# Performance work log

Hardware: AMD Instinct MI355X
Metric: run time of the kernel (lower is better)

The kernel has to match this reference:

```python
import jax, jax.numpy as jnp
import numpy as np


def _trilinear_sample(src, iz, iy, ix):
    """grid_sample 3D, mode='bilinear' (trilinear), padding_mode='zeros', on unnormalized voxel coords.
    src: [B,C,D,H,W]; iz,iy,ix: [B,D,H,W] float voxel coords (iz indexes D, iy H, ix W)."""
    B, C, D, H, W = src.shape
    z0 = jnp.floor(iz); y0 = jnp.floor(iy); x0 = jnp.floor(ix)
    tz = iz - z0; ty = iy - y0; tx = ix - x0
    z0i = z0.astype(jnp.int32); y0i = y0.astype(jnp.int32); x0i = x0.astype(jnp.int32)
    src_flat = src.reshape(B, C, D * H * W)

    def corner(dz, dy, dx):
        zc = z0i + dz; yc = y0i + dy; xc = x0i + dx
        valid = (zc >= 0) & (zc < D) & (yc >= 0) & (yc < H) & (xc >= 0) & (xc < W)
        zcc = jnp.clip(zc, 0, D - 1); ycc = jnp.clip(yc, 0, H - 1); xcc = jnp.clip(xc, 0, W - 1)
        lin = (zcc * H + ycc) * W + xcc                      # [B,D,H,W] flat spatial index
        vals = jax.vmap(lambda v, i: v[:, i.ravel()])(src_flat, lin)  # [B,C,D*H*W]
        vals = vals.reshape(B, C, D, H, W)
        wz = tz if dz else (1.0 - tz)
        wy = ty if dy else (1.0 - ty)
        wx = tx if dx else (1.0 - tx)
        w = (wz * wy * wx) * valid.astype(src.dtype)         # zeros padding
        return vals * w[:, None]

    out = jnp.zeros_like(src)
    for dz in (0, 1):
        for dy in (0, 1):
            for dx in (0, 1):
                out = out + corner(dz, dy, dx)
    return out


def reference(src, flow):
    B, _, D, H, W = flow.shape
    dt = flow.dtype
    # identity grid, channels ordered (z,y,x) i.e. (D,H,W), matching torch.meshgrid indexing='ij'
    gz, gy, gx = jnp.meshgrid(jnp.arange(D, dtype=dt), jnp.arange(H, dtype=dt),
                              jnp.arange(W, dtype=dt), indexing='ij')
    grid = jnp.stack([gz, gy, gx])[None]                     # [1,3,D,H,W]
    coords = grid + flow                                      # absolute voxel coords
    denom = jnp.array([D - 1, H - 1, W - 1], dtype=dt).reshape(1, 3, 1, 1, 1)
    norm = 2.0 * (coords / denom - 0.5)                       # normalized to [-1,1]
    # grid_sample expects last-dim order (x,y,z); align_corners=True unnormalization:
    ix = (norm[:, 2] + 1.0) * (W - 1) * 0.5
    iy = (norm[:, 1] + 1.0) * (H - 1) * 0.5
    iz = (norm[:, 0] + 1.0) * (D - 1) * 0.5
    return _trilinear_sample(src, iz, iy, ix)


def setup_inputs() -> dict:
    key = jax.random.key(0)
    k1, k2 = jax.random.split(key)
    B, C, D, H, W = 2, 2, 128, 160, 128
    src = jax.random.normal(k1, (B, C, D, H, W), dtype=jnp.float32)
    flow = jax.random.normal(k2, (B, 3, D, H, W), dtype=jnp.float32)
    return {"src": src, "flow": flow}
```

## Files before the change

kernel.cpp:

```cpp
#include <hip/hip_runtime.h>


#define B_ 2
#define C_ 2
#define D_ 128
#define H_ 160
#define W_ 128
constexpr int S_ = D_ * H_ * W_;

#define ZT 8
#define YT 8
#define XT 32
#define RZ 3
#define RY 3
#define RX 4
#define CZ (ZT + 2 * RZ)
#define CY (YT + 2 * RY)
#define CX (XT + 2 * RX)
#define NTHREADS 512
#define PLANE (CZ * CY * CX)
#define CHPP (PLANE / 4)
#define NCHUNK_TOT (2 * CHPP)

typedef const __attribute__((address_space(1))) unsigned int ga_u32;
typedef __attribute__((address_space(3))) unsigned int lds_u32;

__device__ __forceinline__ void gload16(const float* g, float* l) {
    __builtin_amdgcn_global_load_lds((ga_u32*)g, (lds_u32*)l, 16, 0, 0);
}

__device__ __forceinline__ float2 compute_pair(
    int x, int y, int z, float fz, float fy, float fx,
    int zb, int yb, int xb,
    int zlo, int zhi, int ylo, int yhi, int xlo, int xhi,
    const float* __restrict__ tile, const float* __restrict__ s0)
{
    const float iz = (float)z + fz;
    const float iy = (float)y + fy;
    const float ix = (float)x + fx;

    const float zf = floorf(iz), yf = floorf(iy), xf = floorf(ix);
    const float tz = iz - zf, ty = iy - yf, tx = ix - xf;
    const int z0 = (int)zf, y0 = (int)yf, x0 = (int)xf;

    const int zc0 = min(max(z0, 0), D_ - 1), zc1 = min(max(z0 + 1, 0), D_ - 1);
    const int yc0 = min(max(y0, 0), H_ - 1), yc1 = min(max(y0 + 1, 0), H_ - 1);
    const int xp  = min(max(x0, 0), W_ - 2);

    const float wz0 = ((unsigned)z0       < (unsigned)D_) ? (1.f - tz) : 0.f;
    const float wz1 = ((unsigned)(z0 + 1) < (unsigned)D_) ? tz         : 0.f;
    const float wy0 = ((unsigned)y0       < (unsigned)H_) ? (1.f - ty) : 0.f;
    const float wy1 = ((unsigned)(y0 + 1) < (unsigned)H_) ? ty         : 0.f;
    const float wx0 = ((unsigned)x0       < (unsigned)W_) ? (1.f - tx) : 0.f;
    const float wx1 = ((unsigned)(x0 + 1) < (unsigned)W_) ? tx         : 0.f;
    const bool hi0 = x0 > xp;
    const bool lo1 = x0 < xp;

    const bool fast = (zc0 >= zlo) & (zc1 < zhi) &
                      (yc0 >= ylo) & (yc1 < yhi) &
                      (xp >= xlo) & (xp + 1 < xhi);

    float acc0, acc1;
    if (fast) {
        const int izl0 = zc0 - (zb - RZ), izl1 = zc1 - (zb - RZ);
        const int iyl0 = yc0 - (yb - RY), iyl1 = yc1 - (yb - RY);
        const int ixl  = xp - (xb - RX);
        const int o00 = (izl0 * CY + iyl0) * CX + ixl;
        const int o01 = (izl0 * CY + iyl1) * CX + ixl;
        const int o10 = (izl1 * CY + iyl0) * CX + ixl;
        const int o11 = (izl1 * CY + iyl1) * CX + ixl;
        const float a00 = tile[o00],         b00 = tile[o00 + 1];
        const float a01 = tile[o01],         b01 = tile[o01 + 1];
        const float a10 = tile[o10],         b10 = tile[o10 + 1];
        const float a11 = tile[o11],         b11 = tile[o11 + 1];
        const float c00 = tile[PLANE + o00], d00 = tile[PLANE + o00 + 1];
        const float c01 = tile[PLANE + o01], d01 = tile[PLANE + o01 + 1];
        const float c10 = tile[PLANE + o10], d10 = tile[PLANE + o10 + 1];
        const float c11 = tile[PLANE + o11], d11 = tile[PLANE + o11 + 1];
        const float q00 = wx0 * (hi0 ? b00 : a00) + wx1 * (lo1 ? a00 : b00);
        const float q01 = wx0 * (hi0 ? b01 : a01) + wx1 * (lo1 ? a01 : b01);
        const float q10 = wx0 * (hi0 ? b10 : a10) + wx1 * (lo1 ? a10 : b10);
        const float q11 = wx0 * (hi0 ? b11 : a11) + wx1 * (lo1 ? a11 : b11);
        const float r00 = wx0 * (hi0 ? d00 : c00) + wx1 * (lo1 ? c00 : d00);
        const float r01 = wx0 * (hi0 ? d01 : c01) + wx1 * (lo1 ? c01 : d01);
        const float r10 = wx0 * (hi0 ? d10 : c10) + wx1 * (lo1 ? c10 : d10);
        const float r11 = wx0 * (hi0 ? d11 : c11) + wx1 * (lo1 ? c11 : d11);
        acc0 = wz0 * (wy0 * q00 + wy1 * q01) + wz1 * (wy0 * q10 + wy1 * q11);
        acc1 = wz0 * (wy0 * r00 + wy1 * r01) + wz1 * (wy0 * r10 + wy1 * r11);
    } else {
        const int l00 = (zc0 * H_ + yc0) * W_ + xp;
        const int l01 = (zc0 * H_ + yc1) * W_ + xp;
        const int l10 = (zc1 * H_ + yc0) * W_ + xp;
        const int l11 = (zc1 * H_ + yc1) * W_ + xp;
        const float a00 = s0[l00],      b00 = s0[l00 + 1];
        const float a01 = s0[l01],      b01 = s0[l01 + 1];
        const float a10 = s0[l10],      b10 = s0[l10 + 1];
        const float a11 = s0[l11],      b11 = s0[l11 + 1];
        const float c00 = s0[S_ + l00], d00 = s0[S_ + l00 + 1];
        const float c01 = s0[S_ + l01], d01 = s0[S_ + l01 + 1];
        const float c10 = s0[S_ + l10], d10 = s0[S_ + l10 + 1];
        const float c11 = s0[S_ + l11], d11 = s0[S_ + l11 + 1];
        const float q00 = wx0 * (hi0 ? b00 : a00) + wx1 * (lo1 ? a00 : b00);
        const float q01 = wx0 * (hi0 ? b01 : a01) + wx1 * (lo1 ? a01 : b01);
        const float q10 = wx0 * (hi0 ? b10 : a10) + wx1 * (lo1 ? a10 : b10);
        const float q11 = wx0 * (hi0 ? b11 : a11) + wx1 * (lo1 ? a11 : b11);
        const float r00 = wx0 * (hi0 ? d00 : c00) + wx1 * (lo1 ? c00 : d00);
        const float r01 = wx0 * (hi0 ? d01 : c01) + wx1 * (lo1 ? c01 : d01);
        const float r10 = wx0 * (hi0 ? d10 : c10) + wx1 * (lo1 ? c10 : d10);
        const float r11 = wx0 * (hi0 ? d11 : c11) + wx1 * (lo1 ? c11 : d11);
        acc0 = wz0 * (wy0 * q00 + wy1 * q01) + wz1 * (wy0 * q10 + wy1 * q11);
        acc1 = wz0 * (wy0 * r00 + wy1 * r01) + wz1 * (wy0 * r10 + wy1 * r11);
    }
    return make_float2(acc0, acc1);
}

__global__ __launch_bounds__(NTHREADS, 4) void warp3d_tile(
    const float* __restrict__ src,
    const float* __restrict__ flow,
    float* __restrict__ out)
{
    __shared__ float tile[2 * PLANE];

    const int tid = threadIdx.x;
    const int xb = blockIdx.x * XT;
    const int yb = blockIdx.y * YT;
    const int bz = blockIdx.z;
    const int zb = (bz & 15) * ZT;
    const int b  = bz >> 4;

    const float* fb = flow + (long long)b * 3 * S_;
    const float* s0 = src + (long long)b * C_ * S_;
    float* o0       = out + (long long)b * C_ * S_;

#pragma unroll
    for (int j = 0; j < 8; ++j) {
        const int lin = j * NTHREADS + tid;
        if (lin < NCHUNK_TOT) {
            const int pl  = (lin >= CHPP) ? 1 : 0;
            const int rem = lin - pl * CHPP;
            const int row = rem / 10;
            const int cq  = rem - row * 10;
            const int rz = row / CY, ry = row - rz * CY;
            const int gz = min(max(zb - RZ + rz, 0), D_ - 1);
            const int gy = min(max(yb - RY + ry, 0), H_ - 1);
            const int gx = min(max(xb - RX + cq * 4, 0), W_ - 4);
            gload16(s0 + pl * S_ + (gz * H_ + gy) * W_ + gx, &tile[lin * 4]);
        }
    }

    const int xq = tid & 7;
    const int ly = (tid >> 3) & 7;
    const int lz = tid >> 6;
    const int x0g = xb + xq * 4;
    const int y = yb + ly, z = zb + lz;
    const int sbase = (z * H_ + y) * W_ + x0g;
    const float4 fz4 = *(const float4*)(fb + sbase);
    const float4 fy4 = *(const float4*)(fb + S_ + sbase);
    const float4 fx4 = *(const float4*)(fb + 2 * S_ + sbase);

    __syncthreads();

    const int zlo = max(0, zb - RZ), zhi = min(D_, zb + ZT + RZ);
    const int ylo = max(0, yb - RY), yhi = min(H_, yb + YT + RY);
    const int xlo = max(0, xb - RX), xhi = min(W_, xb + XT + RX);

    const float2 v0 = compute_pair(x0g + 0, y, z, fz4.x, fy4.x, fx4.x,
                                   zb, yb, xb, zlo, zhi, ylo, yhi, xlo, xhi, tile, s0);
    const float2 v1 = compute_pair(x0g + 1, y, z, fz4.y, fy4.y, fx4.y,
                                   zb, yb, xb, zlo, zhi, ylo, yhi, xlo, xhi, tile, s0);
    const float2 v2 = compute_pair(x0g + 2, y, z, fz4.z, fy4.z, fx4.z,
                                   zb, yb, xb, zlo, zhi, ylo, yhi, xlo, xhi, tile, s0);
    const float2 v3 = compute_pair(x0g + 3, y, z, fz4.w, fy4.w, fx4.w,
                                   zb, yb, xb, zlo, zhi, ylo, yhi, xlo, xhi, tile, s0);

    *(float4*)(o0 + sbase)      = make_float4(v0.x, v1.x, v2.x, v3.x);
    *(float4*)(o0 + S_ + sbase) = make_float4(v0.y, v1.y, v2.y, v3.y);
}

extern "C" void kernel_launch(void* const* d_in, const int* in_sizes, int n_in,
                              void* d_out, int out_size, void* d_ws, size_t ws_size,
                              hipStream_t stream) {
    const float* src  = (const float*)d_in[0];
    const float* flow = (const float*)d_in[1];
    float* out = (float*)d_out;

    dim3 grid(W_ / XT, H_ / YT, (D_ / ZT) * B_);
    warp3d_tile<<<grid, NTHREADS, 0, stream>>>(src, flow, out);
}
```

Baseline: 153.2 us.

## Split channel halo loads and overlap second-channel LDS fill with first-channel compute

The two source channels are now staged into LDS with separate async global-to-LDS batches, each padded to 8192 floats. The kernel waits only for the first channel's batch (and the flow loads), then computes and stores channel 0 while channel 1 is still arriving. The per-voxel setup (weights, offsets, fast-path flag) moves into a shared state struct and is reused across both channels. In exchange it relies on hand-written vmcnt counts that assume in-order completion of memory ops, and it uses slightly more LDS per block.

```diff
diff --git a/kernel.cpp b/kernel.cpp
--- a/kernel.cpp
+++ b/kernel.cpp
@@ -18,9 +18,7 @@
 #define CY (YT + 2 * RY)
 #define CX (XT + 2 * RX)
 #define NTHREADS 512
-#define PLANE (CZ * CY * CX)
-#define CHPP (PLANE / 4)
-#define NCHUNK_TOT (2 * CHPP)
+#define PLANE_PAD 8192
 
 typedef const __attribute__((address_space(1))) unsigned int ga_u32;
 typedef __attribute__((address_space(3))) unsigned int lds_u32;
@@ -29,11 +27,16 @@
     __builtin_amdgcn_global_load_lds((ga_u32*)g, (lds_u32*)l, 16, 0, 0);
 }
 
-__device__ __forceinline__ float2 compute_pair(
+struct PState {
+    int o00, o01, o10, o11;
+    float w00, w01, w10, w11, wx0, wx1;
+    bool hi0, lo1, fast;
+};
+
+__device__ __forceinline__ PState mk_state(
     int x, int y, int z, float fz, float fy, float fx,
     int zb, int yb, int xb,
-    int zlo, int zhi, int ylo, int yhi, int xlo, int xhi,
-    const float* __restrict__ tile, const float* __restrict__ s0)
+    int zlo, int zhi, int ylo, int yhi, int xlo, int xhi)
 {
     const float iz = (float)z + fz;
     const float iy = (float)y + fy;
@@ -51,67 +54,55 @@
     const float wz1 = ((unsigned)(z0 + 1) < (unsigned)D_) ? tz         : 0.f;
     const float wy0 = ((unsigned)y0       < (unsigned)H_) ? (1.f - ty) : 0.f;
     const float wy1 = ((unsigned)(y0 + 1) < (unsigned)H_) ? ty         : 0.f;
-    const float wx0 = ((unsigned)x0       < (unsigned)W_) ? (1.f - tx) : 0.f;
-    const float wx1 = ((unsigned)(x0 + 1) < (unsigned)W_) ? tx         : 0.f;
-    const bool hi0 = x0 > xp;
-    const bool lo1 = x0 < xp;
-
-    const bool fast = (zc0 >= zlo) & (zc1 < zhi) &
-                      (yc0 >= ylo) & (yc1 < yhi) &
-                      (xp >= xlo) & (xp + 1 < xhi);
-
-    float acc0, acc1;
-    if (fast) {
+
+    PState st;
+    st.wx0 = ((unsigned)x0       < (unsigned)W_) ? (1.f - tx) : 0.f;
+    st.wx1 = ((unsigned)(x0 + 1) < (unsigned)W_) ? tx         : 0.f;
+    st.hi0 = x0 > xp;
+    st.lo1 = x0 < xp;
+    st.w00 = wz0 * wy0; st.w01 = wz0 * wy1;
+    st.w10 = wz1 * wy0; st.w11 = wz1 * wy1;
+    st.fast = (zc0 >= zlo) & (zc1 < zhi) &
+              (yc0 >= ylo) & (yc1 < yhi) &
+              (xp >= xlo) & (xp + 1 < xhi);
+    if (st.fast) {
         const int izl0 = zc0 - (zb - RZ), izl1 = zc1 - (zb - RZ);
         const int iyl0 = yc0 - (yb - RY), iyl1 = yc1 - (yb - RY);
         const int ixl  = xp - (xb - RX);
-        const int o00 = (izl0 * CY + iyl0) * CX + ixl;
-        const int o01 = (izl0 * CY + iyl1) * CX + ixl;
-        const int o10 = (izl1 * CY + iyl0) * CX + ixl;
-        const int o11 = (izl1 * CY + iyl1) * CX + ixl;
-        const float a00 = tile[o00],         b00 = tile[o00 + 1];
-        const float a01 = tile[o01],         b01 = tile[o01 + 1];
-        const float a10 = tile[o10],         b10 = tile[o10 + 1];
-        const float a11 = tile[o11],         b11 = tile[o11 + 1];
-        const float c00 = tile[PLANE + o00], d00 = tile[PLANE + o00 + 1];
-        const float c01 = tile[PLANE + o01], d01 = tile[PLANE + o01 + 1];
-        const float c10 = tile[PLANE + o10], d10 = tile[PLANE + o10 + 1];
-        const float c11 = tile[PLANE + o11], d11 = tile[PLANE + o11 + 1];
-        const float q00 = wx0 * (hi0 ? b00 : a00) + wx1 * (lo1 ? a00 : b00);
-        const float q01 = wx0 * (hi0 ? b01 : a01) + wx1 * (lo1 ? a01 : b01);
-        const float q10 = wx0 * (hi0 ? b10 : a10) + wx1 * (lo1 ? a10 : b10);
-        const float q11 = wx0 * (hi0 ? b11 : a11) + wx1 * (lo1 ? a11 : b11);
-        const float r00 = wx0 * (hi0 ? d00 : c00) + wx1 * (lo1 ? c00 : d00);
-        const float r01 = wx0 * (hi0 ? d01 : c01) + wx1 * (lo1 ? c01 : d01);
-        const float r10 = wx0 * (hi0 ? d10 : c10) + wx1 * (lo1 ? c10 : d10);
-        const float r11 = wx0 * (hi0 ? d11 : c11) + wx1 * (lo1 ? c11 : d11);
-        acc0 = wz0 * (wy0 * q00 + wy1 * q01) + wz1 * (wy0 * q10 + wy1 * q11);
-        acc1 = wz0 * (wy0 * r00 + wy1 * r01) + wz1 * (wy0 * r10 + wy1 * r11);
+        st.o00 = (izl0 * CY + iyl0) * CX + ixl;
+        st.o01 = (izl0 * CY + iyl1) * CX + ixl;
+        st.o10 = (izl1 * CY + iyl0) * CX + ixl;
+        st.o11 = (izl1 * CY + iyl1) * CX + ixl;
     } else {
-        const int l00 = (zc0 * H_ + yc0) * W_ + xp;
-        const int l01 = (zc0 * H_ + yc1) * W_ + xp;
-        const int l10 = (zc1 * H_ + yc0) * W_ + xp;
-        const int l11 = (zc1 * H_ + yc1) * W_ + xp;
-        const float a00 = s0[l00],      b00 = s0[l00 + 1];
-        const float a01 = s0[l01],      b01 = s0[l01 + 1];
-        const float a10 = s0[l10],      b10 = s0[l10 + 1];
-        const float a11 = s0[l11],      b11 = s0[l11 + 1];
-        const float c00 = s0[S_ + l00], d00 = s0[S_ + l00 + 1];
-        const float c01 = s0[S_ + l01], d01 = s0[S_ + l01 + 1];
-        const float c10 = s0[S_ + l10], d10 = s0[S_ + l10 + 1];
-        const float c11 = s0[S_ + l11], d11 = s0[S_ + l11 + 1];
-        const float q00 = wx0 * (hi0 ? b00 : a00) + wx1 * (lo1 ? a00 : b00);
-        const float q01 = wx0 * (hi0 ? b01 : a01) + wx1 * (lo1 ? a01 : b01);
-        const float q10 = wx0 * (hi0 ? b10 : a10) + wx1 * (lo1 ? a10 : b10);
-        const float q11 = wx0 * (hi0 ? b11 : a11) + wx1 * (lo1 ? a11 : b11);
-        const float r00 = wx0 * (hi0 ? d00 : c00) + wx1 * (lo1 ? c00 : d00);
-        const float r01 = wx0 * (hi0 ? d01 : c01) + wx1 * (lo1 ? c01 : d01);
-        const float r10 = wx0 * (hi0 ? d10 : c10) + wx1 * (lo1 ? c10 : d10);
-        const float r11 = wx0 * (hi0 ? d11 : c11) + wx1 * (lo1 ? c11 : d11);
-        acc0 = wz0 * (wy0 * q00 + wy1 * q01) + wz1 * (wy0 * q10 + wy1 * q11);
-        acc1 = wz0 * (wy0 * r00 + wy1 * r01) + wz1 * (wy0 * r10 + wy1 * r11);
-    }
-    return make_float2(acc0, acc1);
+        st.o00 = (zc0 * H_ + yc0) * W_ + xp;
+        st.o01 = (zc0 * H_ + yc1) * W_ + xp;
+        st.o10 = (zc1 * H_ + yc0) * W_ + xp;
+        st.o11 = (zc1 * H_ + yc1) * W_ + xp;
+    }
+    return st;
+}
+
+__device__ __forceinline__ float eval_ch(const PState& st,
+                                         const float* __restrict__ ldsp,
+                                         const float* __restrict__ gp)
+{
+    float a00, b00, a01, b01, a10, b10, a11, b11;
+    if (st.fast) {
+        a00 = ldsp[st.o00]; b00 = ldsp[st.o00 + 1];
+        a01 = ldsp[st.o01]; b01 = ldsp[st.o01 + 1];
+        a10 = ldsp[st.o10]; b10 = ldsp[st.o10 + 1];
+        a11 = ldsp[st.o11]; b11 = ldsp[st.o11 + 1];
+    } else {
+        a00 = gp[st.o00]; b00 = gp[st.o00 + 1];
+        a01 = gp[st.o01]; b01 = gp[st.o01 + 1];
+        a10 = gp[st.o10]; b10 = gp[st.o10 + 1];
+        a11 = gp[st.o11]; b11 = gp[st.o11 + 1];
+    }
+    const float q00 = st.wx0 * (st.hi0 ? b00 : a00) + st.wx1 * (st.lo1 ? a00 : b00);
+    const float q01 = st.wx0 * (st.hi0 ? b01 : a01) + st.wx1 * (st.lo1 ? a01 : b01);
+    const float q10 = st.wx0 * (st.hi0 ? b10 : a10) + st.wx1 * (st.lo1 ? a10 : b10);
+    const float q11 = st.wx0 * (st.hi0 ? b11 : a11) + st.wx1 * (st.lo1 ? a11 : b11);
+    return st.w00 * q00 + st.w01 * q01 + st.w10 * q10 + st.w11 * q11;
 }
 
 __global__ __launch_bounds__(NTHREADS, 4) void warp3d_tile(
@@ -119,7 +110,7 @@
     const float* __restrict__ flow,
     float* __restrict__ out)
 {
-    __shared__ float tile[2 * PLANE];
+    __shared__ float tile[2 * PLANE_PAD];
 
     const int tid = threadIdx.x;
     const int xb = blockIdx.x * XT;
@@ -133,19 +124,15 @@
     float* o0       = out + (long long)b * C_ * S_;
 
 #pragma unroll
-    for (int j = 0; j < 8; ++j) {
+    for (int j = 0; j < 4; ++j) {
         const int lin = j * NTHREADS + tid;
-        if (lin < NCHUNK_TOT) {
-            const int pl  = (lin >= CHPP) ? 1 : 0;
-            const int rem = lin - pl * CHPP;
-            const int row = rem / 10;
-            const int cq  = rem - row * 10;
-            const int rz = row / CY, ry = row - rz * CY;
-            const int gz = min(max(zb - RZ + rz, 0), D_ - 1);
-            const int gy = min(max(yb - RY + ry, 0), H_ - 1);
-            const int gx = min(max(xb - RX + cq * 4, 0), W_ - 4);
-            gload16(s0 + pl * S_ + (gz * H_ + gy) * W_ + gx, &tile[lin * 4]);
-        }
+        const int row = lin / 10;
+        const int cq  = lin - row * 10;
+        const int rz = row / CY, ry = row - rz * CY;
+        const int gz = min(max(zb - RZ + rz, 0), D_ - 1);
+        const int gy = min(max(yb - RY + ry, 0), H_ - 1);
+        const int gx = min(max(xb - RX + cq * 4, 0), W_ - 4);
+        gload16(s0 + (gz * H_ + gy) * W_ + gx, &tile[lin * 4]);
     }
 
     const int xq = tid & 7;
@@ -158,23 +145,57 @@
     const float4 fy4 = *(const float4*)(fb + S_ + sbase);
     const float4 fx4 = *(const float4*)(fb + 2 * S_ + sbase);
 
-    __syncthreads();
+    __builtin_amdgcn_sched_barrier(0);
+
+#pragma unroll
+    for (int j = 0; j < 4; ++j) {
+        const int lin = j * NTHREADS + tid;
+        const int row = lin / 10;
+        const int cq  = lin - row * 10;
+        const int rz = row / CY, ry = row - rz * CY;
+        const int gz = min(max(zb - RZ + rz, 0), D_ - 1);
+        const int gy = min(max(yb - RY + ry, 0), H_ - 1);
+        const int gx = min(max(xb - RX + cq * 4, 0), W_ - 4);
+        gload16(s0 + S_ + (gz * H_ + gy) * W_ + gx, &tile[PLANE_PAD + lin * 4]);
+    }
+
+    __builtin_amdgcn_sched_barrier(0);
+
+    asm volatile("s_waitcnt vmcnt(4)" ::: "memory");
+    __builtin_amdgcn_sched_barrier(0);
+    __builtin_amdgcn_s_barrier();
+    __builtin_amdgcn_sched_barrier(0);
 
     const int zlo = max(0, zb - RZ), zhi = min(D_, zb + ZT + RZ);
     const int ylo = max(0, yb - RY), yhi = min(H_, yb + YT + RY);
     const int xlo = max(0, xb - RX), xhi = min(W_, xb + XT + RX);
 
-    const float2 v0 = compute_pair(x0g + 0, y, z, fz4.x, fy4.x, fx4.x,
-                                   zb, yb, xb, zlo, zhi, ylo, yhi, xlo, xhi, tile, s0);
-    const float2 v1 = compute_pair(x0g + 1, y, z, fz4.y, fy4.y, fx4.y,
-                                   zb, yb, xb, zlo, zhi, ylo, yhi, xlo, xhi, tile, s0);
-    const float2 v2 = compute_pair(x0g + 2, y, z, fz4.z, fy4.z, fx4.z,
-                                   zb, yb, xb, zlo, zhi, ylo, yhi, xlo, xhi, tile, s0);
-    const float2 v3 = compute_pair(x0g + 3, y, z, fz4.w, fy4.w, fx4.w,
-                                   zb, yb, xb, zlo, zhi, ylo, yhi, xlo, xhi, tile, s0);
-
-    *(float4*)(o0 + sbase)      = make_float4(v0.x, v1.x, v2.x, v3.x);
-    *(float4*)(o0 + S_ + sbase) = make_float4(v0.y, v1.y, v2.y, v3.y);
+    const PState st0 = mk_state(x0g + 0, y, z, fz4.x, fy4.x, fx4.x,
+                                zb, yb, xb, zlo, zhi, ylo, yhi, xlo, xhi);
+    const PState st1 = mk_state(x0g + 1, y, z, fz4.y, fy4.y, fx4.y,
+                                zb, yb, xb, zlo, zhi, ylo, yhi, xlo, xhi);
+    const PState st2 = mk_state(x0g + 2, y, z, fz4.z, fy4.z, fx4.z,
+                                zb, yb, xb, zlo, zhi, ylo, yhi, xlo, xhi);
+    const PState st3 = mk_state(x0g + 3, y, z, fz4.w, fy4.w, fx4.w,
+                                zb, yb, xb, zlo, zhi, ylo, yhi, xlo, xhi);
+
+    const float c0a = eval_ch(st0, tile, s0);
+    const float c0b = eval_ch(st1, tile, s0);
+    const float c0c = eval_ch(st2, tile, s0);
+    const float c0d = eval_ch(st3, tile, s0);
+
+    asm volatile("s_waitcnt vmcnt(0)" ::: "memory");
+    __builtin_amdgcn_sched_barrier(0);
+    *(float4*)(o0 + sbase) = make_float4(c0a, c0b, c0c, c0d);
+    __builtin_amdgcn_s_barrier();
+    __builtin_amdgcn_sched_barrier(0);
+
+    const float c1a = eval_ch(st0, tile + PLANE_PAD, s0 + S_);
+    const float c1b = eval_ch(st1, tile + PLANE_PAD, s0 + S_);
+    const float c1c = eval_ch(st2, tile + PLANE_PAD, s0 + S_);
+    const float c1d = eval_ch(st3, tile + PLANE_PAD, s0 + S_);
+
+    *(float4*)(o0 + S_ + sbase) = make_float4(c1a, c1b, c1c, c1d);
 }
 
 extern "C" void kernel_launch(void* const* d_in, const int* in_sizes, int n_in,
```

New measurement: 189.1 us. 23.4% more time.

## March blocks along z with double-buffered LDS tiles and prefetched flow

Applied to the files above, without the earlier changes.

Each block now processes four consecutive z-slabs instead of one. While one slab is computed, the next slab's source halo tile is prefetched into a second LDS buffer and its flow vectors into registers, using a manual vmcnt wait and barriers. The intent is to hide global-to-LDS load latency behind the trilinear arithmetic. In exchange, each block uses 128 KB of dynamic LDS, so only one block fits per CU and the grid drops to 640 blocks, which cuts occupancy and risks uneven tail work. The halo is still reloaded in full each step, and the staging loop now also loads padding chunks past the tile.

```diff
diff --git a/kernel.cpp b/kernel.cpp
--- a/kernel.cpp
+++ b/kernel.cpp
@@ -20,20 +20,42 @@
 #define NTHREADS 512
 #define PLANE (CZ * CY * CX)
 #define CHPP (PLANE / 4)
-#define NCHUNK_TOT (2 * CHPP)
+#define BUFFL 16384
+#define ZCHUNK 32
+#define NSTEP (ZCHUNK / ZT)
+#define ZSTRIDE (ZT * H_ * W_)
 
 typedef const __attribute__((address_space(1))) unsigned int ga_u32;
 typedef __attribute__((address_space(3))) unsigned int lds_u32;
 
 __device__ __forceinline__ void gload16(const float* g, float* l) {
     __builtin_amdgcn_global_load_lds((ga_u32*)g, (lds_u32*)l, 16, 0, 0);
+}
+
+__device__ __forceinline__ void stage_tile(const float* __restrict__ s0,
+                                           float* __restrict__ buf,
+                                           int zb, int yb, int xb, int tid)
+{
+#pragma unroll
+    for (int j = 0; j < 8; ++j) {
+        const int lin = j * NTHREADS + tid;
+        const int pl  = (lin >= CHPP) ? 1 : 0;
+        const int rem = lin - pl * CHPP;
+        const int row = rem / 10;
+        const int cq  = rem - row * 10;
+        const int rz = row / CY, ry = row - rz * CY;
+        const int gz = min(max(zb - RZ + rz, 0), D_ - 1);
+        const int gy = min(max(yb - RY + ry, 0), H_ - 1);
+        const int gx = min(max(xb - RX + cq * 4, 0), W_ - 4);
+        gload16(s0 + pl * S_ + (gz * H_ + gy) * W_ + gx, &buf[lin * 4]);
+    }
 }
 
 __device__ __forceinline__ float2 compute_pair(
     int x, int y, int z, float fz, float fy, float fx,
     int zb, int yb, int xb,
     int zlo, int zhi, int ylo, int yhi, int xlo, int xhi,
-    const float* __restrict__ tile, const float* __restrict__ s0)
+    const float* __restrict__ buf, const float* __restrict__ s0)
 {
     const float iz = (float)z + fz;
     const float iy = (float)y + fy;
@@ -69,14 +91,14 @@
         const int o01 = (izl0 * CY + iyl1) * CX + ixl;
         const int o10 = (izl1 * CY + iyl0) * CX + ixl;
         const int o11 = (izl1 * CY + iyl1) * CX + ixl;
-        const float a00 = tile[o00],         b00 = tile[o00 + 1];
-        const float a01 = tile[o01],         b01 = tile[o01 + 1];
-        const float a10 = tile[o10],         b10 = tile[o10 + 1];
-        const float a11 = tile[o11],         b11 = tile[o11 + 1];
-        const float c00 = tile[PLANE + o00], d00 = tile[PLANE + o00 + 1];
-        const float c01 = tile[PLANE + o01], d01 = tile[PLANE + o01 + 1];
-        const float c10 = tile[PLANE + o10], d10 = tile[PLANE + o10 + 1];
-        const float c11 = tile[PLANE + o11], d11 = tile[PLANE + o11 + 1];
+        const float a00 = buf[o00],         b00 = buf[o00 + 1];
+        const float a01 = buf[o01],         b01 = buf[o01 + 1];
+        const float a10 = buf[o10],         b10 = buf[o10 + 1];
+        const float a11 = buf[o11],         b11 = buf[o11 + 1];
+        const float c00 = buf[PLANE + o00], d00 = buf[PLANE + o00 + 1];
+        const float c01 = buf[PLANE + o01], d01 = buf[PLANE + o01 + 1];
+        const float c10 = buf[PLANE + o10], d10 = buf[PLANE + o10 + 1];
+        const float c11 = buf[PLANE + o11], d11 = buf[PLANE + o11 + 1];
         const float q00 = wx0 * (hi0 ? b00 : a00) + wx1 * (lo1 ? a00 : b00);
         const float q01 = wx0 * (hi0 ? b01 : a01) + wx1 * (lo1 ? a01 : b01);
         const float q10 = wx0 * (hi0 ? b10 : a10) + wx1 * (lo1 ? a10 : b10);
@@ -114,67 +136,80 @@
     return make_float2(acc0, acc1);
 }
 
-__global__ __launch_bounds__(NTHREADS, 4) void warp3d_tile(
+__global__ __launch_bounds__(NTHREADS, 2) void warp3d_march(
     const float* __restrict__ src,
     const float* __restrict__ flow,
     float* __restrict__ out)
 {
-    __shared__ float tile[2 * PLANE];
+    extern __shared__ float tile[];
 
     const int tid = threadIdx.x;
     const int xb = blockIdx.x * XT;
     const int yb = blockIdx.y * YT;
     const int bz = blockIdx.z;
-    const int zb = (bz & 15) * ZT;
-    const int b  = bz >> 4;
+    const int zb0 = (bz & 3) * ZCHUNK;
+    const int b   = bz >> 2;
 
     const float* fb = flow + (long long)b * 3 * S_;
     const float* s0 = src + (long long)b * C_ * S_;
     float* o0       = out + (long long)b * C_ * S_;
-
-#pragma unroll
-    for (int j = 0; j < 8; ++j) {
-        const int lin = j * NTHREADS + tid;
-        if (lin < NCHUNK_TOT) {
-            const int pl  = (lin >= CHPP) ? 1 : 0;
-            const int rem = lin - pl * CHPP;
-            const int row = rem / 10;
-            const int cq  = rem - row * 10;
-            const int rz = row / CY, ry = row - rz * CY;
-            const int gz = min(max(zb - RZ + rz, 0), D_ - 1);
-            const int gy = min(max(yb - RY + ry, 0), H_ - 1);
-            const int gx = min(max(xb - RX + cq * 4, 0), W_ - 4);
-            gload16(s0 + pl * S_ + (gz * H_ + gy) * W_ + gx, &tile[lin * 4]);
-        }
-    }
 
     const int xq = tid & 7;
     const int ly = (tid >> 3) & 7;
     const int lz = tid >> 6;
     const int x0g = xb + xq * 4;
-    const int y = yb + ly, z = zb + lz;
-    const int sbase = (z * H_ + y) * W_ + x0g;
-    const float4 fz4 = *(const float4*)(fb + sbase);
-    const float4 fy4 = *(const float4*)(fb + S_ + sbase);
-    const float4 fx4 = *(const float4*)(fb + 2 * S_ + sbase);
-
-    __syncthreads();
-
-    const int zlo = max(0, zb - RZ), zhi = min(D_, zb + ZT + RZ);
+    const int y = yb + ly;
+    int z = zb0 + lz;
+    int sbase = (z * H_ + y) * W_ + x0g;
+
     const int ylo = max(0, yb - RY), yhi = min(H_, yb + YT + RY);
     const int xlo = max(0, xb - RX), xhi = min(W_, xb + XT + RX);
 
-    const float2 v0 = compute_pair(x0g + 0, y, z, fz4.x, fy4.x, fx4.x,
-                                   zb, yb, xb, zlo, zhi, ylo, yhi, xlo, xhi, tile, s0);
-    const float2 v1 = compute_pair(x0g + 1, y, z, fz4.y, fy4.y, fx4.y,
-                                   zb, yb, xb, zlo, zhi, ylo, yhi, xlo, xhi, tile, s0);
-    const float2 v2 = compute_pair(x0g + 2, y, z, fz4.z, fy4.z, fx4.z,
-                                   zb, yb, xb, zlo, zhi, ylo, yhi, xlo, xhi, tile, s0);
-    const float2 v3 = compute_pair(x0g + 3, y, z, fz4.w, fy4.w, fx4.w,
-                                   zb, yb, xb, zlo, zhi, ylo, yhi, xlo, xhi, tile, s0);
-
-    *(float4*)(o0 + sbase)      = make_float4(v0.x, v1.x, v2.x, v3.x);
-    *(float4*)(o0 + S_ + sbase) = make_float4(v0.y, v1.y, v2.y, v3.y);
+    stage_tile(s0, tile, zb0, yb, xb, tid);
+    float4 fzc = *(const float4*)(fb + sbase);
+    float4 fyc = *(const float4*)(fb + S_ + sbase);
+    float4 fxc = *(const float4*)(fb + 2 * S_ + sbase);
+
+#pragma unroll 1
+    for (int t = 0; t < NSTEP; ++t) {
+        const int zb = zb0 + t * ZT;
+        const bool more = (t + 1 < NSTEP);
+        const float* bufc = tile + (t & 1) * BUFFL;
+        float* bufn       = tile + ((t + 1) & 1) * BUFFL;
+
+        if (more) stage_tile(s0, bufn, zb + ZT, yb, xb, tid);
+        const int sbn = sbase + (more ? ZSTRIDE : 0);
+        const float4 fzn = *(const float4*)(fb + sbn);
+        const float4 fyn = *(const float4*)(fb + S_ + sbn);
+        const float4 fxn = *(const float4*)(fb + 2 * S_ + sbn);
+
+        __builtin_amdgcn_sched_barrier(0);
+        if (more) { asm volatile("s_waitcnt vmcnt(11)" ::: "memory"); }
+        else      { asm volatile("s_waitcnt vmcnt(0)"  ::: "memory"); }
+        __builtin_amdgcn_sched_barrier(0);
+        __builtin_amdgcn_s_barrier();
+        __builtin_amdgcn_sched_barrier(0);
+
+        const int zlo = max(0, zb - RZ), zhi = min(D_, zb + ZT + RZ);
+
+        const float2 v0 = compute_pair(x0g + 0, y, z, fzc.x, fyc.x, fxc.x,
+                                       zb, yb, xb, zlo, zhi, ylo, yhi, xlo, xhi, bufc, s0);
+        const float2 v1 = compute_pair(x0g + 1, y, z, fzc.y, fyc.y, fxc.y,
+                                       zb, yb, xb, zlo, zhi, ylo, yhi, xlo, xhi, bufc, s0);
+        const float2 v2 = compute_pair(x0g + 2, y, z, fzc.z, fyc.z, fxc.z,
+                                       zb, yb, xb, zlo, zhi, ylo, yhi, xlo, xhi, bufc, s0);
+        const float2 v3 = compute_pair(x0g + 3, y, z, fzc.w, fyc.w, fxc.w,
+                                       zb, yb, xb, zlo, zhi, ylo, yhi, xlo, xhi, bufc, s0);
+
+        *(float4*)(o0 + sbase)      = make_float4(v0.x, v1.x, v2.x, v3.x);
+        *(float4*)(o0 + S_ + sbase) = make_float4(v0.y, v1.y, v2.y, v3.y);
+
+        __builtin_amdgcn_s_barrier();
+        __builtin_amdgcn_sched_barrier(0);
+
+        fzc = fzn; fyc = fyn; fxc = fxn;
+        sbase = sbn; z += ZT;
+    }
 }
 
 extern "C" void kernel_launch(void* const* d_in, const int* in_sizes, int n_in,
@@ -184,6 +219,14 @@
     const float* flow = (const float*)d_in[1];
     float* out = (float*)d_out;
 
-    dim3 grid(W_ / XT, H_ / YT, (D_ / ZT) * B_);
-    warp3d_tile<<<grid, NTHREADS, 0, stream>>>(src, flow, out);
-}
+    static bool attr_set = false;
+    if (!attr_set) {
+        hipFuncSetAttribute(reinterpret_cast<const void*>(warp3d_march),
+                            hipFuncAttributeMaxDynamicSharedMemorySize,
+                            2 * BUFFL * (int)sizeof(float));
+        attr_set = true;
+    }
+
+    dim3 grid(W_ / XT, H_ / YT, (D_ / ZCHUNK) * B_);
+    warp3d_march<<<grid, NTHREADS, 2 * BUFFL * sizeof(float), stream>>>(src, flow, out);
+}
```

Result: slower. 177.7 us (+16.0%).
